# Performance work log

Measured on AMD Instinct MI355X. Metric: run time of the kernel, lower is better.

The kernel has to match this reference:

```python
import jax, jax.numpy as jnp
import numpy as np
from jax import lax

DIM, HEADS, HIDDEN = 384, 6, 1536
B, D, H, W = 2, 14, 14, 14
LN_EPS = 1e-5


def setup_inputs() -> dict:
    key = jax.random.key(0)
    ks = jax.random.split(key, 8)
    s = 0.02
    return {
        "x": jax.random.normal(ks[0], (B, DIM, D, H, W), jnp.float32),
        "conv_w": jax.random.normal(ks[1], (DIM, 1, 3, 3, 3), jnp.float32) * s,
        "conv_b": jnp.zeros((DIM,), jnp.float32),
        "ln1_w": jnp.ones((DIM,), jnp.float32),
        "ln1_b": jnp.zeros((DIM,), jnp.float32),
        "qkv_w": jax.random.normal(ks[2], (3 * DIM, DIM), jnp.float32) * s,
        "proj_w": jax.random.normal(ks[3], (DIM, DIM), jnp.float32) * s,
        "proj_b": jnp.zeros((DIM,), jnp.float32),
        "ln2_w": jnp.ones((DIM,), jnp.float32),
        "ln2_b": jnp.zeros((DIM,), jnp.float32),
        "fc1_w": jax.random.normal(ks[4], (HIDDEN, DIM), jnp.float32) * s,
        "fc1_b": jnp.zeros((HIDDEN,), jnp.float32),
        "fc2_w": jax.random.normal(ks[5], (DIM, HIDDEN), jnp.float32) * s,
        "fc2_b": jnp.zeros((DIM,), jnp.float32),
    }


def _layernorm(x, w, b):
    mu = jnp.mean(x, axis=-1, keepdims=True)
    var = jnp.var(x, axis=-1, keepdims=True)
    return (x - mu) * lax.rsqrt(var + LN_EPS) * w + b


def reference(x, conv_w, conv_b, ln1_w, ln1_b, qkv_w, proj_w, proj_b,
              ln2_w, ln2_b, fc1_w, fc1_b, fc2_w, fc2_b):
    Bn, C = x.shape[0], x.shape[1]
    Dd, Hh, Ww = x.shape[2], x.shape[3], x.shape[4]
    # depthwise conv3d positional embedding (groups=dim), padding=1
    pos = lax.conv_general_dilated(
        x, conv_w, window_strides=(1, 1, 1), padding="SAME",
        feature_group_count=C,
        dimension_numbers=("NCDHW", "OIDHW", "NCDHW"))
    x = x + pos + conv_b[None, :, None, None, None] * 0 + conv_b[None, :, None, None, None]
    # fix: bias belongs to conv output only once
    x = x - conv_b[None, :, None, None, None]
    N = Dd * Hh * Ww
    t = x.reshape(Bn, C, N).transpose(0, 2, 1)  # [B, N, C]

    # attention
    hd = C // HEADS
    scale = hd ** -0.5
    tn = _layernorm(t, ln1_w, ln1_b)
    qkv = tn @ qkv_w.T  # [B, N, 3C]
    qkv = qkv.reshape(Bn, N, 3, HEADS, hd).transpose(2, 0, 3, 1, 4)
    q, k, v = qkv[0], qkv[1], qkv[2]  # [B, H, N, hd]
    attn = jax.nn.softmax(jnp.einsum("bhnd,bhmd->bhnm", q, k) * scale, axis=-1)
    o = jnp.einsum("bhnm,bhmd->bhnd", attn, v)
    o = o.transpose(0, 2, 1, 3).reshape(Bn, N, C)
    t = t + o @ proj_w.T + proj_b

    # MLP (exact GELU, matching torch nn.GELU default)
    tn2 = _layernorm(t, ln2_w, ln2_b)
    h = jax.nn.gelu(tn2 @ fc1_w.T + fc1_b, approximate=False)
    t = t + h @ fc2_w.T + fc2_b

    return t.transpose(0, 2, 1).reshape(Bn, C, Dd, Hh, Ww)
```

## Files before the change

### kernel.cpp

```cpp
#include <hip/hip_runtime.h>
#include <hip/hip_bf16.h>
#include <math.h>

#define DIM 384
#define HEADS 6
#define HIDDEN 1536
#define NTOK 2744
#define BATCH 2
#define MTOT (BATCH * NTOK)
#define KSPLIT 3
#define NQT 22
#define CEXP 0.18033688f

typedef __bf16 bf16x8 __attribute__((ext_vector_type(8)));
typedef __bf16 bf16x4 __attribute__((ext_vector_type(4)));
typedef float  f32x4  __attribute__((ext_vector_type(4)));

#define F_GELU  1
#define F_RESID 2
#define F_BF16  4
#define F_QKV   8
#define F_TRANS 16

__device__ __forceinline__ void gll16(const void* g, void* l) {
    __builtin_amdgcn_global_load_lds(
        (const __attribute__((address_space(1))) unsigned int*)g,
        (__attribute__((address_space(3))) unsigned int*)l, 16, 0, 0);
}

__global__ void k_conv(const float* __restrict__ x, const float* __restrict__ cw,
                       float* __restrict__ t,
                       const float* __restrict__ w0, const float* __restrict__ w1,
                       const float* __restrict__ w2, const float* __restrict__ w3,
                       __bf16* o0, __bf16* o1, __bf16* o2, __bf16* o3) {
    int bid = blockIdx.x;
    if (bid >= 8448) {
        int i = (bid - 8448) * 256 + threadIdx.x;
        const float* s; __bf16* d; int off;
        if (i < 110592)      { s = w0; d = o0; off = i; }
        else if (i < 147456) { s = w1; d = o1; off = i - 110592; }
        else if (i < 294912) { s = w2; d = o2; off = i - 147456; }
        else                 { s = w3; d = o3; off = i - 294912; }
        float4 v = ((const float4*)s)[off];
        bf16x4 bb = { (__bf16)v.x, (__bf16)v.y, (__bf16)v.z, (__bf16)v.w };
        *(bf16x4*)(d + (size_t)off * 4) = bb;
        return;
    }
    int nb = bid % 11, rest = bid / 11;
    int c = rest % 384, b = rest / 384;
    int n = nb * 256 + threadIdx.x;
    if (n >= NTOK) return;
    int d = n / 196, r = n % 196, h = r / 14, w = r % 14;
    const float* xp = x + ((size_t)b * DIM + c) * NTOK;
    const float* wp = cw + c * 27;
    float acc = xp[n];
    #pragma unroll
    for (int kd = 0; kd < 3; kd++) {
        int dd = d + kd - 1;
        if (dd < 0 || dd >= 14) continue;
        #pragma unroll
        for (int kh = 0; kh < 3; kh++) {
            int hh = h + kh - 1;
            if (hh < 0 || hh >= 14) continue;
            #pragma unroll
            for (int kw = 0; kw < 3; kw++) {
                int ww = w + kw - 1;
                if (ww < 0 || ww >= 14) continue;
                acc += wp[kd * 9 + kh * 3 + kw] * xp[(dd * 14 + hh) * 14 + ww];
            }
        }
    }
    t[((size_t)(b * NTOK + n)) * DIM + c] = acc;
}

__device__ __forceinline__ void ln_body(const float* __restrict__ in,
                                        __bf16* __restrict__ out,
                                        const float* __restrict__ w,
                                        const float* __restrict__ b) {
    int wid = threadIdx.x >> 6, lane = threadIdx.x & 63;
    int token = blockIdx.x * 4 + wid;
    const float* row = in + (size_t)token * DIM;
    float v[6], s = 0.f, s2 = 0.f;
    #pragma unroll
    for (int i = 0; i < 6; i++) {
        v[i] = row[lane + 64 * i];
        s += v[i]; s2 += v[i] * v[i];
    }
    #pragma unroll
    for (int m = 1; m < 64; m <<= 1) { s += __shfl_xor(s, m); s2 += __shfl_xor(s2, m); }
    float mu = s * (1.f / DIM);
    float rstd = rsqrtf(s2 * (1.f / DIM) - mu * mu + 1e-5f);
    __bf16* orow = out + (size_t)token * DIM;
    #pragma unroll
    for (int i = 0; i < 6; i++) {
        int c = lane + 64 * i;
        orow[c] = (__bf16)((v[i] - mu) * rstd * w[c] + b[c]);
    }
}
__global__ void k_ln1(const float* in, __bf16* out, const float* w, const float* b) {
    ln_body(in, out, w, b);
}
__global__ void k_ln2(const float* in, __bf16* out, const float* w, const float* b) {
    ln_body(in, out, w, b);
}

__device__ __forceinline__ void gemm12864_body(
    const __bf16* __restrict__ A, const __bf16* __restrict__ B,
    const float* __restrict__ bias, void* __restrict__ out,
    __bf16* __restrict__ vt_out, int M, int N, int K, int flags) {
    __shared__ __bf16 As[128][64];
    __shared__ __bf16 Bs[64][64];
    int tid = threadIdx.x, lane = tid & 63, wid = tid >> 6;
    int quad = lane >> 4, l16 = lane & 15;
    int wm = wid & 1, wn = wid >> 1;
    int m0 = blockIdx.y * 128, n0 = blockIdx.x * 64;
    int x7 = l16 & 7;

    auto stage = [&](int k0) {
        #pragma unroll
        for (int i = 0; i < 4; i++) {
            int c = i * 256 + tid;
            int row = c >> 3, cc = (c & 7) ^ (row & 7);
            int gm = m0 + row; if (gm > M - 1) gm = M - 1;
            gll16(A + (size_t)gm * K + k0 + cc * 8, &As[0][0] + (size_t)c * 8);
        }
        #pragma unroll
        for (int i = 0; i < 2; i++) {
            int c = i * 256 + tid;
            int row = c >> 3, cc = (c & 7) ^ (row & 7);
            gll16(B + (size_t)(n0 + row) * K + k0 + cc * 8, &Bs[0][0] + (size_t)c * 8);
        }
    };

    f32x4 acc[4][2] = {};
    int nk = K >> 6;
    for (int ki = 0; ki < nk; ki++) {
        if (ki) __syncthreads();
        stage(ki << 6);
        __syncthreads();
        #pragma unroll
        for (int s = 0; s < 2; s++) {
            bf16x8 a[4], b[2];
            #pragma unroll
            for (int i = 0; i < 4; i++)
                a[i] = *(bf16x8*)&As[wm * 64 + i * 16 + l16][(((s * 4 + quad) ^ x7)) * 8];
            #pragma unroll
            for (int j = 0; j < 2; j++)
                b[j] = *(bf16x8*)&Bs[wn * 32 + j * 16 + l16][(((s * 4 + quad) ^ x7)) * 8];
            #pragma unroll
            for (int i = 0; i < 4; i++)
                #pragma unroll
                for (int j = 0; j < 2; j++)
                    acc[i][j] = __builtin_amdgcn_mfma_f32_16x16x32_bf16(a[i], b[j], acc[i][j], 0, 0, 0);
        }
    }

    int colb = n0 + wn * 32;
    #pragma unroll
    for (int j = 0; j < 2; j++) {
        int col = colb + j * 16 + l16;
        float bv = bias ? bias[col] : 0.f;
        #pragma unroll
        for (int i = 0; i < 4; i++) {
            int row0 = m0 + wm * 64 + i * 16 + quad * 4;
            if (row0 >= M) continue;
            float v4[4];
            #pragma unroll
            for (int r = 0; r < 4; r++) {
                float v = acc[i][j][r] + bv;
                if (flags & F_GELU) v = 0.5f * v * (1.f + erff(v * 0.70710678f));
                if ((flags & F_QKV) && col < 384) v *= CEXP;
                v4[r] = v;
            }
            if ((flags & F_QKV) && col >= 768) {
                int b2 = row0 / NTOK, n2 = row0 - b2 * NTOK;
                bf16x4 pk = { (__bf16)v4[0], (__bf16)v4[1], (__bf16)v4[2], (__bf16)v4[3] };
                *(bf16x4*)(vt_out + ((size_t)(b2 * DIM + (col - 768))) * NTOK + n2) = pk;
            } else {
                #pragma unroll
                for (int r = 0; r < 4; r++)
                    ((__bf16*)out)[(size_t)(row0 + r) * N + col] = (__bf16)v4[r];
            }
        }
    }
}
__global__ __launch_bounds__(256) void k_qkv(const __bf16* A, const __bf16* B,
        void* out, __bf16* vt_out, int M, int N, int K) {
    gemm12864_body(A, B, nullptr, out, vt_out, M, N, K, F_QKV);
}
__global__ __launch_bounds__(256) void k_fc1(const __bf16* A, const __bf16* B,
        const float* bias, void* out, int M, int N, int K) {
    gemm12864_body(A, B, bias, out, nullptr, M, N, K, F_GELU | F_BF16);
}

__device__ __forceinline__ void gemm64_body(
    const __bf16* __restrict__ A, const __bf16* __restrict__ B,
    const float* __restrict__ bias, const float* __restrict__ resid,
    void* __restrict__ out, int M, int N, int K, int flags) {
    __shared__ __bf16 As[64][64];
    __shared__ __bf16 Bs[64][64];
    int tid = threadIdx.x, lane = tid & 63, wid = tid >> 6;
    int quad = lane >> 4, l16 = lane & 15;
    int wm = wid & 1, wn = wid >> 1;
    int m0 = blockIdx.y * 64, n0 = blockIdx.x * 64;
    int x7 = l16 & 7;

    auto stage = [&](int k0) {
        #pragma unroll
        for (int i = 0; i < 2; i++) {
            int c = i * 256 + tid;
            int row = c >> 3, cc = (c & 7) ^ (row & 7);
            int gm = m0 + row; if (gm > M - 1) gm = M - 1;
            gll16(A + (size_t)gm * K + k0 + cc * 8, &As[0][0] + (size_t)c * 8);
        }
        #pragma unroll
        for (int i = 0; i < 2; i++) {
            int c = i * 256 + tid;
            int row = c >> 3, cc = (c & 7) ^ (row & 7);
            gll16(B + (size_t)(n0 + row) * K + k0 + cc * 8, &Bs[0][0] + (size_t)c * 8);
        }
    };

    f32x4 acc[2][2] = {};
    int nk = K >> 6;
    for (int ki = 0; ki < nk; ki++) {
        if (ki) __syncthreads();
        stage(ki << 6);
        __syncthreads();
        #pragma unroll
        for (int s = 0; s < 2; s++) {
            bf16x8 a[2], b[2];
            #pragma unroll
            for (int i = 0; i < 2; i++)
                a[i] = *(bf16x8*)&As[wm * 32 + i * 16 + l16][(((s * 4 + quad) ^ x7)) * 8];
            #pragma unroll
            for (int j = 0; j < 2; j++)
                b[j] = *(bf16x8*)&Bs[wn * 32 + j * 16 + l16][(((s * 4 + quad) ^ x7)) * 8];
            #pragma unroll
            for (int i = 0; i < 2; i++)
                #pragma unroll
                for (int j = 0; j < 2; j++)
                    acc[i][j] = __builtin_amdgcn_mfma_f32_16x16x32_bf16(a[i], b[j], acc[i][j], 0, 0, 0);
        }
    }

    #pragma unroll
    for (int j = 0; j < 2; j++) {
        int col = n0 + wn * 32 + j * 16 + l16;
        float bv = bias ? bias[col] : 0.f;
        #pragma unroll
        for (int i = 0; i < 2; i++) {
            int row0 = m0 + wm * 32 + i * 16 + quad * 4;
            if (row0 >= M) continue;
            float v4[4];
            #pragma unroll
            for (int r = 0; r < 4; r++) {
                float v = acc[i][j][r] + bv;
                if (flags & F_RESID) v += resid[(size_t)(row0 + r) * N + col];
                v4[r] = v;
            }
            if (flags & F_TRANS) {
                int b2 = row0 / NTOK, n2 = row0 - b2 * NTOK;
                float4 pk = { v4[0], v4[1], v4[2], v4[3] };
                *(float4*)((float*)out + ((size_t)(b2 * N + col)) * NTOK + n2) = pk;
            } else {
                #pragma unroll
                for (int r = 0; r < 4; r++)
                    ((float*)out)[(size_t)(row0 + r) * N + col] = v4[r];
            }
        }
    }
}
__global__ __launch_bounds__(256) void k_proj(const __bf16* A, const __bf16* B,
        const float* bias, const float* resid, void* out, int M, int N, int K) {
    gemm64_body(A, B, bias, resid, out, M, N, K, F_RESID);
}
__global__ __launch_bounds__(256) void k_fc2(const __bf16* A, const __bf16* B,
        const float* bias, const float* resid, void* out, int M, int N, int K) {
    gemm64_body(A, B, bias, resid, out, M, N, K, F_RESID | F_TRANS);
}

__global__ __launch_bounds__(256) void k_attn(const __bf16* __restrict__ qkv,
                                              const __bf16* __restrict__ vt,
                                              float* __restrict__ opart,
                                              float* __restrict__ lpart) {
    __shared__ __align__(16) char smemQP[128 * 72 * 2];
    __shared__ __bf16 Ks[64][64];
    __shared__ __bf16 Vt[64][64];
    __bf16 (*Qs)[64] = (__bf16(*)[64])smemQP;
    __bf16 (*Ps)[72] = (__bf16(*)[72])smemQP;

    int tid = threadIdx.x, lane = tid & 63, wid = tid >> 6;
    int quad = lane >> 4, l16 = lane & 15;
    int q0 = blockIdx.x * 128;
    int bh = blockIdx.y;
    int ks = blockIdx.z;
    int b = bh / HEADS, h = bh % HEADS;
    int x7 = l16 & 7;

    auto stageKV = [&](int k0) {
        #pragma unroll
        for (int i = 0; i < 2; i++) {
            int c = i * 256 + tid;
            int row = c >> 3, cc = (c & 7) ^ (row & 7);
            int gk = k0 + row; if (gk > NTOK - 1) gk = NTOK - 1;
            gll16(qkv + ((size_t)(b * NTOK + gk)) * 1152 + 384 + h * 64 + cc * 8,
                  &Ks[0][0] + (size_t)c * 8);
            gll16(vt + ((size_t)(bh * 64 + row)) * NTOK + k0 + cc * 8,
                  &Vt[0][0] + (size_t)c * 8);
        }
    };

    int kt0 = (43 * ks) / KSPLIT, kt1 = (43 * (ks + 1)) / KSPLIT;

    #pragma unroll
    for (int i = 0; i < 4; i++) {
        int c = i * 256 + tid;
        int row = c >> 3, cc = (c & 7) ^ (row & 7);
        int gq = q0 + row; if (gq > NTOK - 1) gq = NTOK - 1;
        gll16(qkv + ((size_t)(b * NTOK + gq)) * 1152 + h * 64 + cc * 8,
              &Qs[0][0] + (size_t)c * 8);
    }
    stageKV(kt0 * 64);
    __syncthreads();

    bf16x8 aq[2][2];
    #pragma unroll
    for (int qt = 0; qt < 2; qt++)
        #pragma unroll
        for (int s = 0; s < 2; s++)
            aq[qt][s] = *(bf16x8*)&Qs[wid * 32 + qt * 16 + l16][((s * 4 + quad) ^ x7) * 8];
    __syncthreads();

    f32x4 oacc[2][4] = {};
    float l_part[2][4] = {};
    __bf16* pwr = &Ps[wid * 32 + quad * 4][l16];
    const __bf16* prd = &Ps[wid * 32 + l16][0];

    for (int kt = kt0; kt < kt1; kt++) {
        if (kt > kt0) {
            __syncthreads();
            stageKV(kt * 64);
            __syncthreads();
        }
        int k0 = kt * 64;

        f32x4 s[2][4];
        #pragma unroll
        for (int t = 0; t < 4; t++) {
            bf16x8 bk0 = *(bf16x8*)&Ks[t * 16 + l16][((quad) ^ x7) * 8];
            bf16x8 bk1 = *(bf16x8*)&Ks[t * 16 + l16][((4 + quad) ^ x7) * 8];
            #pragma unroll
            for (int qt = 0; qt < 2; qt++) {
                f32x4 z = {0.f, 0.f, 0.f, 0.f};
                z = __builtin_amdgcn_mfma_f32_16x16x32_bf16(aq[qt][0], bk0, z, 0, 0, 0);
                s[qt][t] = __builtin_amdgcn_mfma_f32_16x16x32_bf16(aq[qt][1], bk1, z, 0, 0, 0);
            }
        }
        if (k0 + 64 > NTOK) {
            #pragma unroll
            for (int t = 0; t < 4; t++)
                if (k0 + t * 16 + l16 >= NTOK)
                    #pragma unroll
                    for (int qt = 0; qt < 2; qt++) {
                        s[qt][t][0] = -1e30f; s[qt][t][1] = -1e30f;
                        s[qt][t][2] = -1e30f; s[qt][t][3] = -1e30f;
                    }
        }
        #pragma unroll
        for (int qt = 0; qt < 2; qt++)
            #pragma unroll
            for (int t = 0; t < 4; t++)
                #pragma unroll
                for (int r = 0; r < 4; r++) {
                    float e = exp2f(s[qt][t][r]);
                    l_part[qt][r] += e;
                    pwr[(qt * 16 + r) * 72 + t * 16] = (__bf16)e;
                }
        bf16x8 ap[2][2];
        #pragma unroll
        for (int qt = 0; qt < 2; qt++)
            #pragma unroll
            for (int sx = 0; sx < 2; sx++)
                ap[qt][sx] = *(bf16x8*)(prd + qt * 16 * 72 + sx * 32 + quad * 8);
        #pragma unroll
        for (int t = 0; t < 4; t++) {
            bf16x8 bv0 = *(bf16x8*)&Vt[t * 16 + l16][((quad) ^ x7) * 8];
            bf16x8 bv1 = *(bf16x8*)&Vt[t * 16 + l16][((4 + quad) ^ x7) * 8];
            #pragma unroll
            for (int qt = 0; qt < 2; qt++) {
                oacc[qt][t] = __builtin_amdgcn_mfma_f32_16x16x32_bf16(ap[qt][0], bv0, oacc[qt][t], 0, 0, 0);
                oacc[qt][t] = __builtin_amdgcn_mfma_f32_16x16x32_bf16(ap[qt][1], bv1, oacc[qt][t], 0, 0, 0);
            }
        }
    }

    #pragma unroll
    for (int qt = 0; qt < 2; qt++)
        #pragma unroll
        for (int r = 0; r < 4; r++) {
            int gq = q0 + wid * 32 + qt * 16 + quad * 4 + r;
            if (gq >= NTOK) continue;
            float l = l_part[qt][r];
            #pragma unroll
            for (int mk = 1; mk < 16; mk <<= 1) l += __shfl_xor(l, mk);
            if (l16 == 0) lpart[((size_t)ks * 12 + bh) * NTOK + gq] = l;
            float* op = opart + ((size_t)ks * MTOT + (size_t)b * NTOK + gq) * DIM + h * 64;
            #pragma unroll
            for (int t = 0; t < 4; t++) op[t * 16 + l16] = oacc[qt][t][r];
        }
}

__global__ void k_comb(const float* __restrict__ opart,
                       const float* __restrict__ lpart,
                       __bf16* __restrict__ o) {
    int idx = blockIdx.x * 256 + threadIdx.x;
    int token = idx / 96, rem = idx - token * 96;
    int c = rem * 4, h = c >> 6;
    int b2 = token / NTOK, n = token - b2 * NTOK;
    int bh = b2 * HEADS + h;
    f32x4 acc = {0.f, 0.f, 0.f, 0.f};
    float l = 0.f;
    #pragma unroll
    for (int ks = 0; ks < KSPLIT; ks++) {
        f32x4 p = *(const f32x4*)&opart[((size_t)ks * MTOT + token) * DIM + c];
        acc[0] += p[0]; acc[1] += p[1]; acc[2] += p[2]; acc[3] += p[3];
        l += lpart[((size_t)ks * 12 + bh) * NTOK + n];
    }
    float inv = 1.f / l;
    bf16x4 ov = { (__bf16)(acc[0] * inv), (__bf16)(acc[1] * inv),
                  (__bf16)(acc[2] * inv), (__bf16)(acc[3] * inv) };
    *(bf16x4*)(o + (size_t)token * DIM + c) = ov;
}

extern "C" void kernel_launch(void* const* d_in, const int* in_sizes, int n_in,
                              void* d_out, int out_size, void* d_ws, size_t ws_size,
                              hipStream_t stream) {
    const float* x      = (const float*)d_in[0];
    const float* conv_w = (const float*)d_in[1];
    const float* ln1_w  = (const float*)d_in[3];
    const float* ln1_b  = (const float*)d_in[4];
    const float* qkv_w  = (const float*)d_in[5];
    const float* proj_w = (const float*)d_in[6];
    const float* proj_b = (const float*)d_in[7];
    const float* ln2_w  = (const float*)d_in[8];
    const float* ln2_b  = (const float*)d_in[9];
    const float* fc1_w  = (const float*)d_in[10];
    const float* fc1_b  = (const float*)d_in[11];
    const float* fc2_w  = (const float*)d_in[12];
    const float* fc2_b  = (const float*)d_in[13];
    float* out = (float*)d_out;

    char* p = (char*)d_ws;
    float*  T    = (float*)p;  p += (size_t)MTOT * DIM * 4;
    __bf16* TN   = (__bf16*)p; p += (size_t)MTOT * DIM * 2;
    __bf16* QKV  = (__bf16*)p; p += (size_t)MTOT * 1152 * 2;
    __bf16* VT   = (__bf16*)p; p += (size_t)BATCH * DIM * NTOK * 2;
    __bf16* O    = (__bf16*)p; p += (size_t)MTOT * DIM * 2;
    __bf16* H    = (__bf16*)p; p += (size_t)MTOT * HIDDEN * 2;
    __bf16* WQ   = (__bf16*)p; p += (size_t)1152 * 384 * 2;
    __bf16* WP   = (__bf16*)p; p += (size_t)384 * 384 * 2;
    __bf16* W1   = (__bf16*)p; p += (size_t)1536 * 384 * 2;
    __bf16* W2   = (__bf16*)p; p += (size_t)384 * 1536 * 2;
    float*  LP   = (float*)p;  p += (size_t)KSPLIT * 12 * NTOK * 4;
    float*  OP   = (float*)p;  p += (size_t)KSPLIT * MTOT * DIM * 4;

    k_conv<<<8448 + 1728, 256, 0, stream>>>(
        x, conv_w, T, qkv_w, proj_w, fc1_w, fc2_w, WQ, WP, W1, W2);
    k_ln1<<<MTOT / 4, 256, 0, stream>>>(T, TN, ln1_w, ln1_b);
    k_qkv<<<dim3(18, 43), 256, 0, stream>>>(TN, WQ, QKV, VT, MTOT, 1152, 384);
    k_attn<<<dim3(NQT, 12, KSPLIT), 256, 0, stream>>>(QKV, VT, OP, LP);
    k_comb<<<(MTOT * 96) / 256, 256, 0, stream>>>(OP, LP, O);
    k_proj<<<dim3(6, 86), 256, 0, stream>>>(O, WP, proj_b, T, T, MTOT, 384, 384);
    k_ln2<<<MTOT / 4, 256, 0, stream>>>(T, TN, ln2_w, ln2_b);
    k_fc1<<<dim3(24, 43), 256, 0, stream>>>(TN, W1, fc1_b, H, MTOT, 1536, 384);
    k_fc2<<<dim3(6, 86), 256, 0, stream>>>(H, W2, fc2_b, T, out, MTOT, 384, 1536);
}
```

Baseline: 249.6 us.

## Coalesce conv and fc2 stores, store attention partials in bf16, raise KSPLIT

Each conv thread now computes 16 channels and writes them as float4s into the token-major buffer, replacing one scattered store per thread. The fc2 epilogue stages its transposed output through shared memory so the NCDHW stores are coalesced. Attention partial outputs are written as bf16 instead of fp32, which halves that traffic and that read in the combine kernel at some precision cost. The attention key split goes from 3 to 4, adding parallelism but also more partials to combine.

```diff
diff --git a/kernel.cpp b/kernel.cpp
--- a/kernel.cpp
+++ b/kernel.cpp
@@ -8,7 +8,7 @@
 #define NTOK 2744
 #define BATCH 2
 #define MTOT (BATCH * NTOK)
-#define KSPLIT 3
+#define KSPLIT 4
 #define NQT 22
 #define CEXP 0.18033688f
 
@@ -34,8 +34,8 @@
                        const float* __restrict__ w2, const float* __restrict__ w3,
                        __bf16* o0, __bf16* o1, __bf16* o2, __bf16* o3) {
     int bid = blockIdx.x;
-    if (bid >= 8448) {
-        int i = (bid - 8448) * 256 + threadIdx.x;
+    if (bid >= 528) {
+        int i = (bid - 528) * 256 + threadIdx.x;
         const float* s; __bf16* d; int off;
         if (i < 110592)      { s = w0; d = o0; off = i; }
         else if (i < 147456) { s = w1; d = o1; off = i - 110592; }
@@ -47,13 +47,15 @@
         return;
     }
     int nb = bid % 11, rest = bid / 11;
-    int c = rest % 384, b = rest / 384;
+    int cb = rest % 24, b = rest / 24;
+    int c0 = cb * 16;
     int n = nb * 256 + threadIdx.x;
     if (n >= NTOK) return;
     int d = n / 196, r = n % 196, h = r / 14, w = r % 14;
-    const float* xp = x + ((size_t)b * DIM + c) * NTOK;
-    const float* wp = cw + c * 27;
-    float acc = xp[n];
+    const float* xb = x + ((size_t)b * DIM + c0) * NTOK;
+    float acc[16];
+    #pragma unroll
+    for (int c = 0; c < 16; c++) acc[c] = xb[(size_t)c * NTOK + n];
     #pragma unroll
     for (int kd = 0; kd < 3; kd++) {
         int dd = d + kd - 1;
@@ -66,11 +68,20 @@
             for (int kw = 0; kw < 3; kw++) {
                 int ww = w + kw - 1;
                 if (ww < 0 || ww >= 14) continue;
-                acc += wp[kd * 9 + kh * 3 + kw] * xp[(dd * 14 + hh) * 14 + ww];
-            }
-        }
-    }
-    t[((size_t)(b * NTOK + n)) * DIM + c] = acc;
+                int np = (dd * 14 + hh) * 14 + ww;
+                int tap = kd * 9 + kh * 3 + kw;
+                #pragma unroll
+                for (int c = 0; c < 16; c++)
+                    acc[c] = fmaf(cw[(c0 + c) * 27 + tap], xb[(size_t)c * NTOK + np], acc[c]);
+            }
+        }
+    }
+    float* tp = t + (size_t)(b * NTOK + n) * DIM + c0;
+    #pragma unroll
+    for (int c = 0; c < 16; c += 4) {
+        float4 v = { acc[c], acc[c + 1], acc[c + 2], acc[c + 3] };
+        *(float4*)(tp + c) = v;
+    }
 }
 
 __device__ __forceinline__ void ln_body(const float* __restrict__ in,
@@ -197,8 +208,10 @@
     const __bf16* __restrict__ A, const __bf16* __restrict__ B,
     const float* __restrict__ bias, const float* __restrict__ resid,
     void* __restrict__ out, int M, int N, int K, int flags) {
-    __shared__ __bf16 As[64][64];
-    __shared__ __bf16 Bs[64][64];
+    __shared__ __align__(16) char sm[17408];
+    __bf16 (*As)[64] = (__bf16(*)[64])sm;
+    __bf16 (*Bs)[64] = (__bf16(*)[64])(sm + 8192);
+    float* Tt = (float*)sm;
     int tid = threadIdx.x, lane = tid & 63, wid = tid >> 6;
     int quad = lane >> 4, l16 = lane & 15;
     int wm = wid & 1, wn = wid >> 1;
@@ -244,6 +257,46 @@
         }
     }
 
+    if (flags & F_TRANS) {
+        #pragma unroll
+        for (int half = 0; half < 2; half++) {
+            __syncthreads();
+            if (wn == half) {
+                #pragma unroll
+                for (int j = 0; j < 2; j++) {
+                    int colL = j * 16 + l16;
+                    int col = n0 + half * 32 + colL;
+                    float bv = bias[col];
+                    #pragma unroll
+                    for (int i = 0; i < 2; i++) {
+                        int rowL = wm * 32 + i * 16 + quad * 4;
+                        float v4[4];
+                        #pragma unroll
+                        for (int r = 0; r < 4; r++) {
+                            int rr = m0 + rowL + r; if (rr > M - 1) rr = M - 1;
+                            v4[r] = acc[i][j][r] + bv + resid[(size_t)rr * N + col];
+                        }
+                        float4 pk = { v4[0], v4[1], v4[2], v4[3] };
+                        *(float4*)&Tt[colL * 68 + rowL] = pk;
+                    }
+                }
+            }
+            __syncthreads();
+            int c = tid >> 3, no = (tid & 7) * 8;
+            int col = n0 + half * 32 + c;
+            #pragma unroll
+            for (int q2 = 0; q2 < 2; q2++) {
+                int nn = no + q2 * 4;
+                int row = m0 + nn;
+                if (row >= M) continue;
+                int b2 = row / NTOK, n2 = row - b2 * NTOK;
+                float4 v = *(float4*)&Tt[c * 68 + nn];
+                *(float4*)((float*)out + ((size_t)(b2 * N + col)) * NTOK + n2) = v;
+            }
+        }
+        return;
+    }
+
     #pragma unroll
     for (int j = 0; j < 2; j++) {
         int col = n0 + wn * 32 + j * 16 + l16;
@@ -252,21 +305,11 @@
         for (int i = 0; i < 2; i++) {
             int row0 = m0 + wm * 32 + i * 16 + quad * 4;
             if (row0 >= M) continue;
-            float v4[4];
             #pragma unroll
             for (int r = 0; r < 4; r++) {
                 float v = acc[i][j][r] + bv;
                 if (flags & F_RESID) v += resid[(size_t)(row0 + r) * N + col];
-                v4[r] = v;
-            }
-            if (flags & F_TRANS) {
-                int b2 = row0 / NTOK, n2 = row0 - b2 * NTOK;
-                float4 pk = { v4[0], v4[1], v4[2], v4[3] };
-                *(float4*)((float*)out + ((size_t)(b2 * N + col)) * NTOK + n2) = pk;
-            } else {
-                #pragma unroll
-                for (int r = 0; r < 4; r++)
-                    ((float*)out)[(size_t)(row0 + r) * N + col] = v4[r];
+                ((float*)out)[(size_t)(row0 + r) * N + col] = v;
             }
         }
     }
@@ -282,7 +325,7 @@
 
 __global__ __launch_bounds__(256) void k_attn(const __bf16* __restrict__ qkv,
                                               const __bf16* __restrict__ vt,
-                                              float* __restrict__ opart,
+                                              __bf16* __restrict__ opart,
                                               float* __restrict__ lpart) {
     __shared__ __align__(16) char smemQP[128 * 72 * 2];
     __shared__ __bf16 Ks[64][64];
@@ -405,13 +448,13 @@
             #pragma unroll
             for (int mk = 1; mk < 16; mk <<= 1) l += __shfl_xor(l, mk);
             if (l16 == 0) lpart[((size_t)ks * 12 + bh) * NTOK + gq] = l;
-            float* op = opart + ((size_t)ks * MTOT + (size_t)b * NTOK + gq) * DIM + h * 64;
-            #pragma unroll
-            for (int t = 0; t < 4; t++) op[t * 16 + l16] = oacc[qt][t][r];
-        }
-}
-
-__global__ void k_comb(const float* __restrict__ opart,
+            __bf16* op = opart + ((size_t)ks * MTOT + (size_t)b * NTOK + gq) * DIM + h * 64;
+            #pragma unroll
+            for (int t = 0; t < 4; t++) op[t * 16 + l16] = (__bf16)oacc[qt][t][r];
+        }
+}
+
+__global__ void k_comb(const __bf16* __restrict__ opart,
                        const float* __restrict__ lpart,
                        __bf16* __restrict__ o) {
     int idx = blockIdx.x * 256 + threadIdx.x;
@@ -419,17 +462,16 @@
     int c = rem * 4, h = c >> 6;
     int b2 = token / NTOK, n = token - b2 * NTOK;
     int bh = b2 * HEADS + h;
-    f32x4 acc = {0.f, 0.f, 0.f, 0.f};
-    float l = 0.f;
+    float a0 = 0.f, a1 = 0.f, a2 = 0.f, a3 = 0.f, l = 0.f;
     #pragma unroll
     for (int ks = 0; ks < KSPLIT; ks++) {
-        f32x4 p = *(const f32x4*)&opart[((size_t)ks * MTOT + token) * DIM + c];
-        acc[0] += p[0]; acc[1] += p[1]; acc[2] += p[2]; acc[3] += p[3];
+        bf16x4 p = *(const bf16x4*)&opart[((size_t)ks * MTOT + token) * DIM + c];
+        a0 += (float)p[0]; a1 += (float)p[1]; a2 += (float)p[2]; a3 += (float)p[3];
         l += lpart[((size_t)ks * 12 + bh) * NTOK + n];
     }
     float inv = 1.f / l;
-    bf16x4 ov = { (__bf16)(acc[0] * inv), (__bf16)(acc[1] * inv),
-                  (__bf16)(acc[2] * inv), (__bf16)(acc[3] * inv) };
+    bf16x4 ov = { (__bf16)(a0 * inv), (__bf16)(a1 * inv),
+                  (__bf16)(a2 * inv), (__bf16)(a3 * inv) };
     *(bf16x4*)(o + (size_t)token * DIM + c) = ov;
 }
 
@@ -463,9 +505,9 @@
     __bf16* W1   = (__bf16*)p; p += (size_t)1536 * 384 * 2;
     __bf16* W2   = (__bf16*)p; p += (size_t)384 * 1536 * 2;
     float*  LP   = (float*)p;  p += (size_t)KSPLIT * 12 * NTOK * 4;
-    float*  OP   = (float*)p;  p += (size_t)KSPLIT * MTOT * DIM * 4;
-
-    k_conv<<<8448 + 1728, 256, 0, stream>>>(
+    __bf16* OP   = (__bf16*)p; p += (size_t)KSPLIT * MTOT * DIM * 2;
+
+    k_conv<<<528 + 1728, 256, 0, stream>>>(
         x, conv_w, T, qkv_w, proj_w, fc1_w, fc2_w, WQ, WP, W1, W2);
     k_ln1<<<MTOT / 4, 256, 0, stream>>>(T, TN, ln1_w, ln1_b);
     k_qkv<<<dim3(18, 43), 256, 0, stream>>>(TN, WQ, QKV, VT, MTOT, 1152, 384);
```

Result: faster. 231.2 us (-7.4%).
